# Kernel tuning notes

Hardware: AMD Instinct MI355X
Metric: run time of the kernel (lower is better)

The kernel has to match this reference:

```python
import jax, jax.numpy as jnp
import numpy as np

B = 8192   # batch / node count
D = 1024   # feature dim
K = 20     # k nearest neighbors (k+1 = 21 edges per row incl. self)


def setup_inputs() -> dict:
    key = jax.random.key(0)
    k1, k2 = jax.random.split(key)
    x = jax.random.normal(k1, (B, D), dtype=jnp.float32)
    # nn.init.normal_(edge_weights, mean=1.0, std=0.01)
    edge_weights = 1.0 + 0.01 * jax.random.normal(k2, (K + 1,), dtype=jnp.float32)
    return {"x": x, "edge_weights": edge_weights}


def reference(x, edge_weights):
    # F.normalize(x, p=2, dim=1): divide by max(||x||, eps)
    norm = jnp.maximum(jnp.linalg.norm(x, axis=1, keepdims=True), 1e-12)
    xn = x / norm
    adj = xn @ xn.T                                  # [B, B] cosine similarity
    _, idx = jax.lax.top_k(adj, K + 1)               # [B, K+1] neighbor indices
    rows = jnp.arange(B)[:, None]                    # [B, 1]
    # scatter learned per-rank edge weights; topk indices are distinct per row,
    # so set() matches the torch per-rank assignment loop (mask is redundant).
    w = jnp.zeros((B, B), dtype=x.dtype).at[rows, idx].set(
        jnp.broadcast_to(edge_weights, (B, K + 1))
    )
    row_sum = w.sum(axis=1, keepdims=True) + 1e-8
    return w / row_sum
```

## Files before the change

### kernel.cpp

```cpp
#include <hip/hip_runtime.h>
#include <hip/hip_bf16.h>
#include <float.h>
#include <math.h>

#define B_N 8192
#define D_N 1024
#define KP1 21
#define THRESH0 0.07f
#define MARGIN 1.5e-3f
#define CAND_CAP 64
#define SURV_CAP 256

typedef __attribute__((ext_vector_type(8))) short short8;
typedef __attribute__((ext_vector_type(4))) float floatx4;

__device__ __forceinline__ unsigned short f32_to_bf16_rtne(float f) {
    unsigned int u = __float_as_uint(f);
    unsigned int r = (u + 0x7FFFu + ((u >> 16) & 1u)) >> 16;
    return (unsigned short)r;
}

__device__ __forceinline__ void async_copy16(const void* g, void* l) {
    __builtin_amdgcn_global_load_lds(
        (const __attribute__((address_space(1))) void*)g,
        (__attribute__((address_space(3))) void*)l, 16, 0, 0);
}

__global__ __launch_bounds__(256) void normalize_kernel(const float* __restrict__ x,
                                                        float* __restrict__ xn32,
                                                        unsigned short* __restrict__ xbf) {
    int row = blockIdx.x;
    int t = threadIdx.x;
    const float* xr = x + (size_t)row * D_N;
    float v[4];
#pragma unroll
    for (int m = 0; m < 4; ++m) v[m] = xr[t + 256 * m];
    double s = 0.0;
#pragma unroll
    for (int m = 0; m < 4; ++m) { double d = (double)v[m]; s += d * d; }
#pragma unroll
    for (int off = 32; off > 0; off >>= 1) s += __shfl_down(s, off, 64);
    __shared__ double p[4];
    if ((t & 63) == 0) p[t >> 6] = s;
    __syncthreads();
    double nrm = sqrt(p[0] + p[1] + p[2] + p[3]);
    if (nrm < 1e-12) nrm = 1e-12;
    float* xo = xn32 + (size_t)row * D_N;
    unsigned short* xb = xbf + (size_t)row * D_N;
#pragma unroll
    for (int m = 0; m < 4; ++m) {
        float q = (float)((double)v[m] / nrm);
        xo[t + 256 * m] = q;
        xb[t + 256 * m] = f32_to_bf16_rtne(q);
    }
}

__global__ __launch_bounds__(256) void mfma_gemm_kernel(const unsigned short* __restrict__ xb,
                                                        unsigned short* __restrict__ gram) {
    __shared__ unsigned char smem[33280];
    int i = blockIdx.x;
    int by = (int)((129.0f - sqrtf(16641.0f - 8.0f * (float)i)) * 0.5f);
    while (by > 0 && by * (129 - by) / 2 > i) --by;
    while ((by + 1) * (128 - by) / 2 <= i) ++by;
    int bx = by + (i - by * (129 - by) / 2);

    unsigned char* As = smem;
    unsigned char* Bs = smem + 16384;
    const int t = threadIdx.x;
    const int lane = t & 63;
    const int w = t >> 6;
    const int wr = w >> 1, wc = w & 1;
    const char* Ag = (const char*)xb + (size_t)(by * 128) * 2048;
    const char* Bg = (const char*)xb + (size_t)(bx * 128) * 2048;

    int goff[4], loff[4];
#pragma unroll
    for (int q = 0; q < 4; ++q) {
        int e = w * 4 + q;
        int r = e * 8 + (lane >> 3);
        int ch = (lane & 7) ^ (lane >> 3);
        goff[q] = r * 2048 + ch * 16;
        loff[q] = e * 1024;
    }

    int kc = lane >> 4, rl = lane & 15;
    int aoff[2][4], boff[2][4];
#pragma unroll
    for (int s = 0; s < 2; ++s)
#pragma unroll
        for (int ii = 0; ii < 4; ++ii) {
            int a_r = wr * 64 + ii * 16 + rl;
            aoff[s][ii] = a_r * 128 + (((s * 4 + kc) ^ (rl & 7)) << 4);
            int b_r = wc * 64 + ii * 16 + rl;
            boff[s][ii] = b_r * 128 + (((s * 4 + kc) ^ (rl & 7)) << 4);
        }

    floatx4 acc[4][4] = {};
    for (int kb = 0; kb < D_N; kb += 64) {
        int koff = kb * 2;
#pragma unroll
        for (int q = 0; q < 4; ++q) async_copy16(Ag + goff[q] + koff, As + loff[q]);
#pragma unroll
        for (int q = 0; q < 4; ++q) async_copy16(Bg + goff[q] + koff, Bs + loff[q]);
        __syncthreads();
#pragma unroll
        for (int s = 0; s < 2; ++s) {
            short8 af[4], bfv[4];
#pragma unroll
            for (int ii = 0; ii < 4; ++ii) af[ii] = *(const short8*)(As + aoff[s][ii]);
#pragma unroll
            for (int ii = 0; ii < 4; ++ii) bfv[ii] = *(const short8*)(Bs + boff[s][ii]);
#pragma unroll
            for (int mi = 0; mi < 4; ++mi)
#pragma unroll
                for (int nj = 0; nj < 4; ++nj)
                    acc[mi][nj] = __builtin_amdgcn_mfma_f32_16x16x32_bf16(af[mi], bfv[nj], acc[mi][nj], 0, 0, 0);
        }
        __syncthreads();
    }

    int lrow = wr * 64 + (lane >> 4) * 4;
    int lcol = wc * 64 + (lane & 15);
    unsigned short* tile = (unsigned short*)smem;
#pragma unroll
    for (int mi = 0; mi < 4; ++mi)
#pragma unroll
        for (int nj = 0; nj < 4; ++nj)
#pragma unroll
            for (int e = 0; e < 4; ++e)
                tile[(lrow + mi * 16 + e) * 130 + lcol + nj * 16] = f32_to_bf16_rtne(acc[mi][nj][e]);
    __syncthreads();

    int rt = t >> 4;
    int cb = (t & 15) * 8;
    uint4* ntile = (uint4*)(gram + ((size_t)(by * 64 + bx) << 14));
#pragma unroll
    for (int c = 0; c < 8; ++c) {
        int r = c * 16 + rt;
        unsigned short v[8];
#pragma unroll
        for (int ii = 0; ii < 8; ++ii) v[ii] = tile[r * 130 + cb + ii];
        ntile[c * 256 + t] = *(const uint4*)v;
    }
    if (bx != by) {
        uint4* ttile = (uint4*)(gram + ((size_t)(bx * 64 + by) << 14));
#pragma unroll
        for (int c = 0; c < 8; ++c) {
            int r = c * 16 + rt;
            unsigned short v[8];
#pragma unroll
            for (int s = 0; s < 8; ++s) {
                int ii = (s + (lane >> 2)) & 7;
                v[ii] = tile[(cb + ii) * 130 + r];
            }
            ttile[c * 256 + t] = *(const uint4*)v;
        }
    }
}

__global__ __launch_bounds__(256) void compact_rescore_out_kernel(const unsigned short* __restrict__ gram,
                                                                  const float* __restrict__ xn32,
                                                                  const float* __restrict__ ew,
                                                                  float* __restrict__ out) {
    __shared__ float4 xi4[D_N / 4];
    __shared__ unsigned int skey[SURV_CAP];
    __shared__ int scol[SURV_CAP];
    __shared__ int hist1[256];
    __shared__ int hist2[256];
    __shared__ int cidx[CAND_CAP];
    __shared__ double ssc[CAND_CAP];
    __shared__ int sid[CAND_CAP];
    __shared__ int widx[KP1];
    __shared__ float wval[KP1];
    __shared__ int scnt, ccnt, key21s;
    int row = blockIdx.x, t = threadIdx.x;
    int lane = t & 63, w = t >> 6;

    xi4[t] = ((const float4*)(xn32 + (size_t)row * D_N))[t];
    hist1[t] = 0;
    if (t < CAND_CAP) { ssc[t] = -DBL_MAX; sid[t] = 0x7FFFFFFF; }
    if (t == 0) { scnt = 0; ccnt = 0; key21s = 0; }
    __syncthreads();

    const uint4* grow = (const uint4*)gram + (size_t)(row >> 7) * 64 * 2048 + (size_t)(row & 127) * 16;
#pragma unroll
    for (int m = 0; m < 4; ++m) {
        int g = t + 256 * m;
        uint4 pr = grow[(size_t)(g >> 4) * 2048 + (g & 15)];
        unsigned int w4[4] = {pr.x, pr.y, pr.z, pr.w};
        int base = ((g >> 4) << 7) + ((g & 15) << 3);
#pragma unroll
        for (int q = 0; q < 4; ++q) {
            unsigned int k0 = w4[q] & 0xFFFFu;
            unsigned int k1 = w4[q] >> 16;
            float v0 = __uint_as_float(k0 << 16);
            float v1 = __uint_as_float(k1 << 16);
            if (v0 > THRESH0) {
                int p = atomicAdd(&scnt, 1);
                if (p < SURV_CAP) { skey[p] = k0; scol[p] = base + q * 2; atomicAdd(&hist1[k0 >> 8], 1); }
            }
            if (v1 > THRESH0) {
                int p = atomicAdd(&scnt, 1);
                if (p < SURV_CAP) { skey[p] = k1; scol[p] = base + q * 2 + 1; atomicAdd(&hist1[k1 >> 8], 1); }
            }
        }
    }
    __syncthreads();
    int sc = scnt < SURV_CAP ? scnt : SURV_CAP;

    if (w == 0) {
        int h0 = hist1[4 * lane], h1 = hist1[4 * lane + 1], h2 = hist1[4 * lane + 2], h3 = hist1[4 * lane + 3];
        int sl = h0 + h1 + h2 + h3;
        int v = sl;
#pragma unroll
        for (int off = 1; off < 64; off <<= 1) {
            int u = __shfl_down(v, off, 64);
            if (lane + off < 64) v += u;
        }
        int E = v - sl;
        int T3 = E, T2 = E + h3, T1 = T2 + h2, Tc0 = T1 + h1;
        int Hl = -1, Rl = 0;
        if      (T3  < KP1 && KP1 <= T3  + h3) { Hl = 4 * lane + 3; Rl = KP1 - T3; }
        else if (T2  < KP1 && KP1 <= T2  + h2) { Hl = 4 * lane + 2; Rl = KP1 - T2; }
        else if (T1  < KP1 && KP1 <= T1  + h1) { Hl = 4 * lane + 1; Rl = KP1 - T1; }
        else if (Tc0 < KP1 && KP1 <= Tc0 + h0) { Hl = 4 * lane;     Rl = KP1 - Tc0; }
        unsigned long long bal = __ballot(Hl >= 0);
        if (bal) {
            int src = __ffsll((long long)bal) - 1;
            int H = __shfl(Hl, src, 64);
            int R = __shfl(Rl, src, 64);
#pragma unroll
            for (int ii = 0; ii < 4; ++ii) hist2[4 * lane + ii] = 0;
#pragma unroll
            for (int r = 0; r < 4; ++r) {
                int s = lane + 64 * r;
                if (s < sc) {
                    unsigned int k = skey[s];
                    if ((int)(k >> 8) == H) atomicAdd(&hist2[k & 255], 1);
                }
            }
            int g0 = hist2[4 * lane], g1 = hist2[4 * lane + 1], g2 = hist2[4 * lane + 2], g3 = hist2[4 * lane + 3];
            int sl2 = g0 + g1 + g2 + g3;
            int v2 = sl2;
#pragma unroll
            for (int off = 1; off < 64; off <<= 1) {
                int u = __shfl_down(v2, off, 64);
                if (lane + off < 64) v2 += u;
            }
            int E2 = v2 - sl2;
            int U3 = E2, U2 = E2 + g3, U1 = U2 + g2, Uc0 = U1 + g1;
            int Ll = -1;
            if      (U3  < R && R <= U3  + g3) Ll = 4 * lane + 3;
            else if (U2  < R && R <= U2  + g2) Ll = 4 * lane + 2;
            else if (U1  < R && R <= U1  + g1) Ll = 4 * lane + 1;
            else if (Uc0 < R && R <= Uc0 + g0) Ll = 4 * lane;
            if (Ll >= 0) key21s = (H << 8) | Ll;
        }
    }
    __syncthreads();

    float v21 = __uint_as_float((unsigned int)key21s << 16);
    float cutoff = v21 - MARGIN;
    if (t < sc) {
        float vf = __uint_as_float(skey[t] << 16);
        if (vf >= cutoff) {
            int p = atomicAdd(&ccnt, 1);
            if (p < CAND_CAP) cidx[p] = scol[t];
        }
    }
    __syncthreads();
    int count = ccnt < CAND_CAP ? ccnt : CAND_CAP;

    for (int c = w; c < count; c += 4) {
        int j = cidx[c];
        if (j >= 0 && j < B_N) {
            const float4* xj4 = (const float4*)(xn32 + (size_t)j * D_N);
            double s = 0.0;
#pragma unroll
            for (int m = 0; m < 4; ++m) {
                float4 a = xi4[lane + 64 * m];
                float4 b = xj4[lane + 64 * m];
                s = fma((double)a.x, (double)b.x, s);
                s = fma((double)a.y, (double)b.y, s);
                s = fma((double)a.z, (double)b.z, s);
                s = fma((double)a.w, (double)b.w, s);
            }
#pragma unroll
            for (int off = 32; off > 0; off >>= 1) s += __shfl_down(s, off, 64);
            if (lane == 0) { ssc[c] = s; sid[c] = j; }
        }
    }
    __syncthreads();

    if (w == 0) {
        double mv = ssc[lane];
        int mi = sid[lane];
#pragma unroll
        for (int k = 2; k <= 64; k <<= 1) {
#pragma unroll
            for (int j = 32; j > 0; j >>= 1) {
                if (j < k) {
                    double ov = __shfl_xor(mv, j, 64);
                    int oi = __shfl_xor(mi, j, 64);
                    bool iLower = (lane & j) == 0;
                    bool dirDesc = (lane & k) == 0;
                    bool other_first = (ov > mv) || (ov == mv && oi < mi);
                    bool take = (iLower == dirDesc) ? other_first : !other_first;
                    if (take) { mv = ov; mi = oi; }
                }
            }
        }
        if (lane < KP1) {
            double s = 1e-8;
#pragma unroll
            for (int k = 0; k < KP1; ++k) s += (double)ew[k];
            widx[lane] = mi;
            wval[lane] = (float)((double)ew[lane] / s);
        }
    }
    __syncthreads();

    float* orow = out + (size_t)row * B_N;
    float4* orow4 = (float4*)orow;
    float4 z = make_float4(0.f, 0.f, 0.f, 0.f);
#pragma unroll
    for (int m = 0; m < 8; ++m) orow4[t + 256 * m] = z;
    __syncthreads();
    if (t < KP1) {
        int c = widx[t];
        if (c >= 0 && c < B_N) orow[c] = wval[t];
    }
}

extern "C" void kernel_launch(void* const* d_in, const int* in_sizes, int n_in,
                              void* d_out, int out_size, void* d_ws, size_t ws_size,
                              hipStream_t stream) {
    const float* x = (const float*)d_in[0];
    const float* ew = (const float*)d_in[1];

    unsigned short* gram = (unsigned short*)d_ws;
    float* xn32 = (float*)((char*)d_ws + ((size_t)128 << 20));
    unsigned short* xbf = (unsigned short*)((char*)d_ws + ((size_t)160 << 20));

    normalize_kernel<<<B_N, 256, 0, stream>>>(x, xn32, xbf);
    mfma_gemm_kernel<<<2080, 256, 0, stream>>>(xbf, gram);
    compact_rescore_out_kernel<<<B_N, 256, 0, stream>>>(gram, xn32, ew, (float*)d_out);
}
```

Before: 508.4 us.

## Process two rows per block and issue output zeroing and loads upfront

The compact/rescore kernel now handles two adjacent rows per block, halving the grid. It zeroes both output rows at kernel start and preloads both rows' gram data and normalized vectors into registers and LDS before the sequential selection work, so the streaming stores and loads can overlap with the histogram and rescoring phases. The edge-weight sum is hoisted out of the per-row loop. In exchange, per-block register and LDS use rises and each block runs two serial selection passes, which lowers parallelism per row.

```diff
diff --git a/kernel.cpp b/kernel.cpp
--- a/kernel.cpp
+++ b/kernel.cpp
@@ -162,7 +162,7 @@
                                                                   const float* __restrict__ xn32,
                                                                   const float* __restrict__ ew,
                                                                   float* __restrict__ out) {
-    __shared__ float4 xi4[D_N / 4];
+    __shared__ float4 xia[2][D_N / 4];
     __shared__ unsigned int skey[SURV_CAP];
     __shared__ int scol[SURV_CAP];
     __shared__ int hist1[256];
@@ -173,162 +173,179 @@
     __shared__ int widx[KP1];
     __shared__ float wval[KP1];
     __shared__ int scnt, ccnt, key21s;
-    int row = blockIdx.x, t = threadIdx.x;
+    int t = threadIdx.x;
     int lane = t & 63, w = t >> 6;
-
-    xi4[t] = ((const float4*)(xn32 + (size_t)row * D_N))[t];
-    hist1[t] = 0;
-    if (t < CAND_CAP) { ssc[t] = -DBL_MAX; sid[t] = 0x7FFFFFFF; }
-    if (t == 0) { scnt = 0; ccnt = 0; key21s = 0; }
-    __syncthreads();
-
-    const uint4* grow = (const uint4*)gram + (size_t)(row >> 7) * 64 * 2048 + (size_t)(row & 127) * 16;
+    int row0 = blockIdx.x * 2;
+
+    float* orowA = out + (size_t)row0 * B_N;
+    float4 z = make_float4(0.f, 0.f, 0.f, 0.f);
+    float4* oA4 = (float4*)orowA;
+#pragma unroll
+    for (int m = 0; m < 16; ++m) oA4[t + 256 * m] = z;
+
+    const uint4* grow0 = (const uint4*)gram + (size_t)(row0 >> 7) * 64 * 2048 + (size_t)(row0 & 127) * 16;
+    const uint4* grow1 = grow0 + 16;
+    uint4 pr0[4], pr1[4];
 #pragma unroll
     for (int m = 0; m < 4; ++m) {
         int g = t + 256 * m;
-        uint4 pr = grow[(size_t)(g >> 4) * 2048 + (g & 15)];
-        unsigned int w4[4] = {pr.x, pr.y, pr.z, pr.w};
-        int base = ((g >> 4) << 7) + ((g & 15) << 3);
-#pragma unroll
-        for (int q = 0; q < 4; ++q) {
-            unsigned int k0 = w4[q] & 0xFFFFu;
-            unsigned int k1 = w4[q] >> 16;
-            float v0 = __uint_as_float(k0 << 16);
-            float v1 = __uint_as_float(k1 << 16);
-            if (v0 > THRESH0) {
-                int p = atomicAdd(&scnt, 1);
-                if (p < SURV_CAP) { skey[p] = k0; scol[p] = base + q * 2; atomicAdd(&hist1[k0 >> 8], 1); }
-            }
-            if (v1 > THRESH0) {
-                int p = atomicAdd(&scnt, 1);
-                if (p < SURV_CAP) { skey[p] = k1; scol[p] = base + q * 2 + 1; atomicAdd(&hist1[k1 >> 8], 1); }
-            }
-        }
-    }
-    __syncthreads();
-    int sc = scnt < SURV_CAP ? scnt : SURV_CAP;
-
-    if (w == 0) {
-        int h0 = hist1[4 * lane], h1 = hist1[4 * lane + 1], h2 = hist1[4 * lane + 2], h3 = hist1[4 * lane + 3];
-        int sl = h0 + h1 + h2 + h3;
-        int v = sl;
-#pragma unroll
-        for (int off = 1; off < 64; off <<= 1) {
-            int u = __shfl_down(v, off, 64);
-            if (lane + off < 64) v += u;
-        }
-        int E = v - sl;
-        int T3 = E, T2 = E + h3, T1 = T2 + h2, Tc0 = T1 + h1;
-        int Hl = -1, Rl = 0;
-        if      (T3  < KP1 && KP1 <= T3  + h3) { Hl = 4 * lane + 3; Rl = KP1 - T3; }
-        else if (T2  < KP1 && KP1 <= T2  + h2) { Hl = 4 * lane + 2; Rl = KP1 - T2; }
-        else if (T1  < KP1 && KP1 <= T1  + h1) { Hl = 4 * lane + 1; Rl = KP1 - T1; }
-        else if (Tc0 < KP1 && KP1 <= Tc0 + h0) { Hl = 4 * lane;     Rl = KP1 - Tc0; }
-        unsigned long long bal = __ballot(Hl >= 0);
-        if (bal) {
-            int src = __ffsll((long long)bal) - 1;
-            int H = __shfl(Hl, src, 64);
-            int R = __shfl(Rl, src, 64);
-#pragma unroll
-            for (int ii = 0; ii < 4; ++ii) hist2[4 * lane + ii] = 0;
-#pragma unroll
-            for (int r = 0; r < 4; ++r) {
-                int s = lane + 64 * r;
-                if (s < sc) {
-                    unsigned int k = skey[s];
-                    if ((int)(k >> 8) == H) atomicAdd(&hist2[k & 255], 1);
-                }
-            }
-            int g0 = hist2[4 * lane], g1 = hist2[4 * lane + 1], g2 = hist2[4 * lane + 2], g3 = hist2[4 * lane + 3];
-            int sl2 = g0 + g1 + g2 + g3;
-            int v2 = sl2;
+        pr0[m] = grow0[(size_t)(g >> 4) * 2048 + (g & 15)];
+        pr1[m] = grow1[(size_t)(g >> 4) * 2048 + (g & 15)];
+    }
+    xia[0][t] = ((const float4*)(xn32 + (size_t)row0 * D_N))[t];
+    xia[1][t] = ((const float4*)(xn32 + (size_t)(row0 + 1) * D_N))[t];
+
+    double ews = 1e-8;
+#pragma unroll
+    for (int k = 0; k < KP1; ++k) ews += (double)ew[k];
+
+#pragma unroll
+    for (int rr = 0; rr < 2; ++rr) {
+        int row = row0 + rr;
+        float* orow = out + (size_t)row * B_N;
+        const float4* xi4 = xia[rr];
+
+        hist1[t] = 0;
+        if (t < CAND_CAP) { ssc[t] = -DBL_MAX; sid[t] = 0x7FFFFFFF; }
+        if (t == 0) { scnt = 0; ccnt = 0; key21s = 0; }
+        __syncthreads();
+
+#pragma unroll
+        for (int m = 0; m < 4; ++m) {
+            uint4 pr = rr ? pr1[m] : pr0[m];
+            unsigned int w4[4] = {pr.x, pr.y, pr.z, pr.w};
+            int g = t + 256 * m;
+            int base = ((g >> 4) << 7) + ((g & 15) << 3);
+#pragma unroll
+            for (int q = 0; q < 4; ++q) {
+                unsigned int k0 = w4[q] & 0xFFFFu;
+                unsigned int k1 = w4[q] >> 16;
+                float v0 = __uint_as_float(k0 << 16);
+                float v1 = __uint_as_float(k1 << 16);
+                if (v0 > THRESH0) {
+                    int p = atomicAdd(&scnt, 1);
+                    if (p < SURV_CAP) { skey[p] = k0; scol[p] = base + q * 2; atomicAdd(&hist1[k0 >> 8], 1); }
+                }
+                if (v1 > THRESH0) {
+                    int p = atomicAdd(&scnt, 1);
+                    if (p < SURV_CAP) { skey[p] = k1; scol[p] = base + q * 2 + 1; atomicAdd(&hist1[k1 >> 8], 1); }
+                }
+            }
+        }
+        __syncthreads();
+        int sc = scnt < SURV_CAP ? scnt : SURV_CAP;
+
+        if (w == 0) {
+            int h0 = hist1[4 * lane], h1 = hist1[4 * lane + 1], h2 = hist1[4 * lane + 2], h3 = hist1[4 * lane + 3];
+            int sl = h0 + h1 + h2 + h3;
+            int v = sl;
 #pragma unroll
             for (int off = 1; off < 64; off <<= 1) {
-                int u = __shfl_down(v2, off, 64);
-                if (lane + off < 64) v2 += u;
-            }
-            int E2 = v2 - sl2;
-            int U3 = E2, U2 = E2 + g3, U1 = U2 + g2, Uc0 = U1 + g1;
-            int Ll = -1;
-            if      (U3  < R && R <= U3  + g3) Ll = 4 * lane + 3;
-            else if (U2  < R && R <= U2  + g2) Ll = 4 * lane + 2;
-            else if (U1  < R && R <= U1  + g1) Ll = 4 * lane + 1;
-            else if (Uc0 < R && R <= Uc0 + g0) Ll = 4 * lane;
-            if (Ll >= 0) key21s = (H << 8) | Ll;
-        }
-    }
-    __syncthreads();
-
-    float v21 = __uint_as_float((unsigned int)key21s << 16);
-    float cutoff = v21 - MARGIN;
-    if (t < sc) {
-        float vf = __uint_as_float(skey[t] << 16);
-        if (vf >= cutoff) {
-            int p = atomicAdd(&ccnt, 1);
-            if (p < CAND_CAP) cidx[p] = scol[t];
-        }
-    }
-    __syncthreads();
-    int count = ccnt < CAND_CAP ? ccnt : CAND_CAP;
-
-    for (int c = w; c < count; c += 4) {
-        int j = cidx[c];
-        if (j >= 0 && j < B_N) {
-            const float4* xj4 = (const float4*)(xn32 + (size_t)j * D_N);
-            double s = 0.0;
-#pragma unroll
-            for (int m = 0; m < 4; ++m) {
-                float4 a = xi4[lane + 64 * m];
-                float4 b = xj4[lane + 64 * m];
-                s = fma((double)a.x, (double)b.x, s);
-                s = fma((double)a.y, (double)b.y, s);
-                s = fma((double)a.z, (double)b.z, s);
-                s = fma((double)a.w, (double)b.w, s);
-            }
-#pragma unroll
-            for (int off = 32; off > 0; off >>= 1) s += __shfl_down(s, off, 64);
-            if (lane == 0) { ssc[c] = s; sid[c] = j; }
-        }
-    }
-    __syncthreads();
-
-    if (w == 0) {
-        double mv = ssc[lane];
-        int mi = sid[lane];
-#pragma unroll
-        for (int k = 2; k <= 64; k <<= 1) {
-#pragma unroll
-            for (int j = 32; j > 0; j >>= 1) {
-                if (j < k) {
-                    double ov = __shfl_xor(mv, j, 64);
-                    int oi = __shfl_xor(mi, j, 64);
-                    bool iLower = (lane & j) == 0;
-                    bool dirDesc = (lane & k) == 0;
-                    bool other_first = (ov > mv) || (ov == mv && oi < mi);
-                    bool take = (iLower == dirDesc) ? other_first : !other_first;
-                    if (take) { mv = ov; mi = oi; }
-                }
-            }
-        }
-        if (lane < KP1) {
-            double s = 1e-8;
-#pragma unroll
-            for (int k = 0; k < KP1; ++k) s += (double)ew[k];
-            widx[lane] = mi;
-            wval[lane] = (float)((double)ew[lane] / s);
-        }
-    }
-    __syncthreads();
-
-    float* orow = out + (size_t)row * B_N;
-    float4* orow4 = (float4*)orow;
-    float4 z = make_float4(0.f, 0.f, 0.f, 0.f);
-#pragma unroll
-    for (int m = 0; m < 8; ++m) orow4[t + 256 * m] = z;
-    __syncthreads();
-    if (t < KP1) {
-        int c = widx[t];
-        if (c >= 0 && c < B_N) orow[c] = wval[t];
+                int u = __shfl_down(v, off, 64);
+                if (lane + off < 64) v += u;
+            }
+            int E = v - sl;
+            int T3 = E, T2 = E + h3, T1 = T2 + h2, Tc0 = T1 + h1;
+            int Hl = -1, Rl = 0;
+            if      (T3  < KP1 && KP1 <= T3  + h3) { Hl = 4 * lane + 3; Rl = KP1 - T3; }
+            else if (T2  < KP1 && KP1 <= T2  + h2) { Hl = 4 * lane + 2; Rl = KP1 - T2; }
+            else if (T1  < KP1 && KP1 <= T1  + h1) { Hl = 4 * lane + 1; Rl = KP1 - T1; }
+            else if (Tc0 < KP1 && KP1 <= Tc0 + h0) { Hl = 4 * lane;     Rl = KP1 - Tc0; }
+            unsigned long long bal = __ballot(Hl >= 0);
+            if (bal) {
+                int src = __ffsll((long long)bal) - 1;
+                int H = __shfl(Hl, src, 64);
+                int R = __shfl(Rl, src, 64);
+#pragma unroll
+                for (int ii = 0; ii < 4; ++ii) hist2[4 * lane + ii] = 0;
+#pragma unroll
+                for (int r = 0; r < 4; ++r) {
+                    int s = lane + 64 * r;
+                    if (s < sc) {
+                        unsigned int k = skey[s];
+                        if ((int)(k >> 8) == H) atomicAdd(&hist2[k & 255], 1);
+                    }
+                }
+                int g0 = hist2[4 * lane], g1 = hist2[4 * lane + 1], g2 = hist2[4 * lane + 2], g3 = hist2[4 * lane + 3];
+                int sl2 = g0 + g1 + g2 + g3;
+                int v2 = sl2;
+#pragma unroll
+                for (int off = 1; off < 64; off <<= 1) {
+                    int u = __shfl_down(v2, off, 64);
+                    if (lane + off < 64) v2 += u;
+                }
+                int E2 = v2 - sl2;
+                int U3 = E2, U2 = E2 + g3, U1 = U2 + g2, Uc0 = U1 + g1;
+                int Ll = -1;
+                if      (U3  < R && R <= U3  + g3) Ll = 4 * lane + 3;
+                else if (U2  < R && R <= U2  + g2) Ll = 4 * lane + 2;
+                else if (U1  < R && R <= U1  + g1) Ll = 4 * lane + 1;
+                else if (Uc0 < R && R <= Uc0 + g0) Ll = 4 * lane;
+                if (Ll >= 0) key21s = (H << 8) | Ll;
+            }
+        }
+        __syncthreads();
+
+        float v21 = __uint_as_float((unsigned int)key21s << 16);
+        float cutoff = v21 - MARGIN;
+        if (t < sc) {
+            float vf = __uint_as_float(skey[t] << 16);
+            if (vf >= cutoff) {
+                int p = atomicAdd(&ccnt, 1);
+                if (p < CAND_CAP) cidx[p] = scol[t];
+            }
+        }
+        __syncthreads();
+        int count = ccnt < CAND_CAP ? ccnt : CAND_CAP;
+
+        for (int c = w; c < count; c += 4) {
+            int j = cidx[c];
+            if (j >= 0 && j < B_N) {
+                const float4* xj4 = (const float4*)(xn32 + (size_t)j * D_N);
+                double s = 0.0;
+#pragma unroll
+                for (int m = 0; m < 4; ++m) {
+                    float4 a = xi4[lane + 64 * m];
+                    float4 b = xj4[lane + 64 * m];
+                    s = fma((double)a.x, (double)b.x, s);
+                    s = fma((double)a.y, (double)b.y, s);
+                    s = fma((double)a.z, (double)b.z, s);
+                    s = fma((double)a.w, (double)b.w, s);
+                }
+#pragma unroll
+                for (int off = 32; off > 0; off >>= 1) s += __shfl_down(s, off, 64);
+                if (lane == 0) { ssc[c] = s; sid[c] = j; }
+            }
+        }
+        __syncthreads();
+
+        if (w == 0) {
+            double mv = ssc[lane];
+            int mi = sid[lane];
+#pragma unroll
+            for (int k = 2; k <= 64; k <<= 1) {
+#pragma unroll
+                for (int j = 32; j > 0; j >>= 1) {
+                    if (j < k) {
+                        double ov = __shfl_xor(mv, j, 64);
+                        int oi = __shfl_xor(mi, j, 64);
+                        bool iLower = (lane & j) == 0;
+                        bool dirDesc = (lane & k) == 0;
+                        bool other_first = (ov > mv) || (ov == mv && oi < mi);
+                        bool take = (iLower == dirDesc) ? other_first : !other_first;
+                        if (take) { mv = ov; mi = oi; }
+                    }
+                }
+            }
+            if (lane < KP1) { widx[lane] = mi; wval[lane] = (float)((double)ew[lane] / ews); }
+        }
+        __syncthreads();
+
+        if (t < KP1) {
+            int c = widx[t];
+            if (c >= 0 && c < B_N) orow[c] = wval[t];
+        }
+        __syncthreads();
     }
 }
 
@@ -344,5 +361,5 @@
 
     normalize_kernel<<<B_N, 256, 0, stream>>>(x, xn32, xbf);
     mfma_gemm_kernel<<<2080, 256, 0, stream>>>(xbf, gram);
-    compact_rescore_out_kernel<<<B_N, 256, 0, stream>>>(gram, xn32, ew, (float*)d_out);
-}
+    compact_rescore_out_kernel<<<B_N / 2, 256, 0, stream>>>(gram, xn32, ew, (float*)d_out);
+}
```

Result: no change. 511.6 us (+0.6%).
